# Kernel tuning notes

Hardware: AMD Instinct MI355X
Metric: run time of the kernel (lower is better)

Reference implementation:

```python
import jax, jax.numpy as jnp
import numpy as np
from jax import lax

NUM_ITER = 10
SMOOTH = 1.0
CL_WEIGHT = 0.5


def _min_pool(x, wh, ww):
    # torch: -max_pool2d(-x) pads with -inf -> min-pool with +inf boundary
    return lax.reduce_window(x, jnp.inf, lax.min,
                             (1, 1, wh, ww), (1, 1, 1, 1),
                             [(0, 0), (0, 0), (wh // 2, wh // 2), (ww // 2, ww // 2)])


def _max_pool(x, wh, ww):
    return lax.reduce_window(x, -jnp.inf, lax.max,
                             (1, 1, wh, ww), (1, 1, 1, 1),
                             [(0, 0), (0, 0), (wh // 2, wh // 2), (ww // 2, ww // 2)])


def soft_erode(img):
    return jnp.minimum(_min_pool(img, 3, 1), _min_pool(img, 1, 3))


def soft_dilate(img):
    return _max_pool(img, 3, 3)


def soft_open(img):
    return soft_dilate(soft_erode(img))


def soft_skeleton(img, num_iter=NUM_ITER):
    # img: (B,1,H,W)
    skel = jax.nn.relu(img - soft_open(img))

    def body(i, carry):
        img_e, skel = carry
        img_e = soft_erode(img_e)
        delta = jax.nn.relu(img_e - soft_open(img_e))
        skel = skel + jax.nn.relu(delta - skel * delta)
        return (img_e, skel)

    _, skel = lax.fori_loop(0, num_iter, body, (img, skel))
    return skel


def soft_dice(pred, target, smooth=SMOOTH):
    inter = jnp.sum(pred * target)
    return (2.0 * inter + smooth) / (jnp.sum(pred) + jnp.sum(target) + smooth)


def setup_inputs() -> dict:
    key = jax.random.key(0)
    k1, k2 = jax.random.split(key)
    pred = jax.random.normal(k1, (8, 1, 1024, 1024), dtype=jnp.float32)
    target = jax.random.randint(k2, (8, 1, 1024, 1024), 0, 2, dtype=jnp.int32)
    return {"pred": pred, "target": target}


def reference(pred, target):
    pred_prob = jax.nn.sigmoid(pred)          # (B,1,H,W)
    target_f = target.astype(pred_prob.dtype)

    skel_pred = soft_skeleton(pred_prob)
    skel_target = soft_skeleton(target_f)

    tprec = (jnp.sum(skel_pred * target_f) + SMOOTH) / (jnp.sum(skel_pred) + SMOOTH)
    tsens = (jnp.sum(skel_target * pred_prob) + SMOOTH) / (jnp.sum(skel_target) + SMOOTH)
    cl_dice = 2.0 * tprec * tsens / (tprec + tsens + 1e-7)

    dice = soft_dice(pred_prob, target_f)
    combined = (1.0 - CL_WEIGHT) * dice + CL_WEIGHT * cl_dice
    loss = 1.0 - combined
    return loss
```

## Files before the change

### kernel.cpp

```cpp
#include <hip/hip_runtime.h>
#include <math.h>

#define IMG  1024
#define TILE 64
#define HALO 12
#define SPP  52
#define NPRED (90*SPP)
#define SEN2 0x40004000u

typedef _Float16 h2 __attribute__((ext_vector_type(2)));
union UH { unsigned u; h2 h; };
__device__ __forceinline__ h2 u2h(unsigned u){ UH x; x.u=u; return x.h; }
__device__ __forceinline__ unsigned h2u(h2 h){ UH x; x.h=h; return x.u; }
__device__ __forceinline__ h2 pmin(h2 a, h2 b){ return __builtin_elementwise_min(a,b); }
__device__ __forceinline__ h2 pmax(h2 a, h2 b){ return __builtin_elementwise_max(a,b); }
__device__ __forceinline__ h2 funnel(h2 hi_src, h2 lo_src){
  return u2h((h2u(lo_src)>>16) | (h2u(hi_src)<<16));
}
__device__ __forceinline__ float sigmoidf(float x){ return 1.0f/(1.0f+__expf(-x)); }
__device__ __forceinline__ h2 unsent(h2 x, h2 onev, h2 zerov){
  h2 t = pmax(x-onev, zerov); return x - t - t;
}
__device__ __forceinline__ unsigned extract8(unsigned w0, unsigned w1, unsigned w2, int bp){
  unsigned long long lo = (unsigned long long)w0 | ((unsigned long long)w1<<32);
  unsigned long long hi = (unsigned long long)w1 | ((unsigned long long)w2<<32);
  unsigned a = (unsigned)(lo >> bp);
  unsigned b = (unsigned)(hi >> (bp & 31));
  return ((bp < 32) ? a : b) & 0xFFu;
}
__device__ __forceinline__ uint4 erode5(uint4 rm, uint4 rc, uint4 rn, h2 lw, h2 rv){
  h2 a0=u2h(rc.x), a1=u2h(rc.y), a2=u2h(rc.z), a3=u2h(rc.w);
  h2 v0=pmin(u2h(rm.x), u2h(rn.x));
  h2 v1=pmin(u2h(rm.y), u2h(rn.y));
  h2 v2=pmin(u2h(rm.z), u2h(rn.z));
  h2 v3=pmin(u2h(rm.w), u2h(rn.w));
  h2 f0=funnel(a0,lw), f1=funnel(a1,a0), f2=funnel(a2,a1), f3=funnel(a3,a2), f4=funnel(rv,a3);
  uint4 e;
  e.x=h2u(pmin(pmin(f0,f1),pmin(v0,a0)));
  e.y=h2u(pmin(pmin(f1,f2),pmin(v1,a1)));
  e.z=h2u(pmin(pmin(f2,f3),pmin(v2,a2)));
  e.w=h2u(pmin(pmin(f3,f4),pmin(v3,a3)));
  return e;
}

template<bool BND>
__device__ void pipeline(const float* __restrict__ pred, const int* __restrict__ targ,
                         long base, int gr0, int gc0, int tid,
                         unsigned* P, unsigned* Ta,
                         h2 val[8], h2 skel[8], unsigned &tbits, unsigned &skbits) {
  for (int i = tid; i < 104; i += 256) {
    int r = (i < 52) ? 0 : 89, c = (i < 52) ? i : i - 52;
    P[r*SPP + c] = SEN2;
  }
  for (int i = tid; i < 704; i += 256) {
    int r = 1 + (i >> 3), w = i & 7;
    w = (w < 2) ? w : 44 + w;
    P[r*SPP + w] = SEN2;
  }
  if (!BND) {
    #pragma unroll
    for (int k=0;k<4;++k){
      int u = tid + (k<<8);
      if (u < 968){
        int r = u/11, q = u - r*11;
        long g = base + (long)(gr0+r)*IMG + gc0 + (q<<3);
        float4 pa = *(const float4*)(pred+g);
        float4 pb = *(const float4*)(pred+g+4);
        h2 w0 = {(_Float16)sigmoidf(pa.x), (_Float16)sigmoidf(pa.y)};
        h2 w1 = {(_Float16)sigmoidf(pa.z), (_Float16)sigmoidf(pa.w)};
        h2 w2 = {(_Float16)sigmoidf(pb.x), (_Float16)sigmoidf(pb.y)};
        h2 w3 = {(_Float16)sigmoidf(pb.z), (_Float16)sigmoidf(pb.w)};
        int o = (1+r)*SPP + 2 + (q<<2);
        uint2 d0; d0.x=h2u(w0); d0.y=h2u(w1);
        uint2 d1; d1.x=h2u(w2); d1.y=h2u(w3);
        *(uint2*)&P[o]   = d0;
        *(uint2*)&P[o+2] = d1;
      }
    }
    #pragma unroll
    for (int k=0;k<2;++k){
      int u = tid + (k<<8);
      if (u < 264){
        int r = u/3, w = u - r*3;
        long g = base + (long)(gr0+r)*IMG + gc0 + (w<<5);
        unsigned bits = 0;
        #pragma unroll
        for (int i=0;i<8;++i){
          if (w < 2 || i < 6) {
            int4 tv = *(const int4*)(targ + g + (i<<2));
            unsigned nib = (unsigned)(tv.x!=0) | ((unsigned)(tv.y!=0)<<1)
                         | ((unsigned)(tv.z!=0)<<2) | ((unsigned)(tv.w!=0)<<3);
            bits |= nib << (i<<2);
          }
        }
        if (w==2) bits |= 0xFF000000u;
        Ta[u] = bits;
      }
    }
  } else {
    for (int i=tid; i<88*44; i+=256){
      int r = i/44, wd = i - r*44;
      int gr = gr0 + r;
      bool rok = (unsigned)gr < (unsigned)IMG;
      int gca = gc0 + (wd<<1), gcb = gca + 1;
      _Float16 va = (_Float16)2.0f, vb = (_Float16)2.0f;
      if (rok && (unsigned)gca < (unsigned)IMG) va = (_Float16)sigmoidf(pred[base + (long)gr*IMG + gca]);
      if (rok && (unsigned)gcb < (unsigned)IMG) vb = (_Float16)sigmoidf(pred[base + (long)gr*IMG + gcb]);
      h2 w; w.x = va; w.y = vb;
      P[(1+r)*SPP + 2 + wd] = h2u(w);
    }
    for (int u=tid; u<264; u+=256){
      int r = u/3, w = u - r*3;
      int gr = gr0 + r;
      bool rok = (unsigned)gr < (unsigned)IMG;
      unsigned bits = 0;
      for (int b=0;b<32;++b){
        int c = (w<<5) + b;
        unsigned bit = 1;
        if (c < 88) {
          int gc = gc0 + c;
          if (rok && (unsigned)gc < (unsigned)IMG) bit = (unsigned)(targ[base+(long)gr*IMG+gc] != 0);
        }
        bits |= bit << b;
      }
      Ta[u] = bits;
    }
  }
  __syncthreads();

  unsigned cm0=~0u, cm1=~0u, cm2=0x00FFFFFFu;
  bool colO = false;
  if (BND) {
    int lo = (-gc0 > 0) ? -gc0 : 0;
    int hi = (IMG - gc0 < 88) ? (IMG - gc0) : 88;
    colO = (lo > 0) || (hi < 88);
    unsigned m[3];
    #pragma unroll
    for (int w=0; w<3; ++w){
      int l = lo - (w<<5); if (l<0) l=0;
      int h = hi - (w<<5); if (h>32) h=32;
      unsigned mm = 0;
      if (h > l) {
        unsigned top = (h>=32)? ~0u : ((1u<<h)-1u);
        unsigned bot = (l<=0)? 0u : ((1u<<l)-1u);
        mm = top & ~bot;
      }
      m[w]=mm;
    }
    cm0=m[0]; cm1=m[1]; cm2=m[2] & 0x00FFFFFF;
  }

  const bool eact0 = (tid < 216);
  const int es = tid / 12, eq = tid - es*12;
  const int s5 = es * 5;
  const int ew = eq << 2;
  const int to = 3 + tid;
  const int twd = tid - (tid/3)*3;
  const bool tex = (tid < 2);
  const int to2 = 259 + tid;
  const int twd2 = (256+tid) - ((256+tid)/3)*3;

  const int qc = tid & 7;
  const int rg = tid >> 3;
  const int r0 = HALO + (rg<<1);
  const int wq = 8 + (qc<<2);
  const int bp = 12 + (qc<<3);

  h2 ep[8];
  {
    uint4 a0 = *(const uint4*)&P[(r0+1)*SPP + wq];
    uint4 a1 = *(const uint4*)&P[(r0+2)*SPP + wq];
    ep[0]=u2h(a0.x); ep[1]=u2h(a0.y); ep[2]=u2h(a0.z); ep[3]=u2h(a0.w);
    ep[4]=u2h(a1.x); ep[5]=u2h(a1.y); ep[6]=u2h(a1.z); ep[7]=u2h(a1.w);
    #pragma unroll
    for (int i=0;i<8;++i){ val[i]=ep[i]; skel[i]=(h2)(_Float16)0.0f; }
  }
  {
    int oa = r0*3, ob = (r0+1)*3;
    tbits = extract8(Ta[oa],Ta[oa+1],Ta[oa+2],bp)
          | (extract8(Ta[ob],Ta[ob+1],Ta[ob+2],bp) << 8);
  }
  unsigned tp0=0,tp1=0,tp2=0, sk0=0,sk1=0,sk2=0;
  const bool td = (tid < 64);
  const int tro = (12 + tid)*3;
  if (td) { tp0=Ta[tro]; tp1=Ta[tro+1]; tp2=Ta[tro+2]; }

  const h2 onev  = {(_Float16)1.0f,(_Float16)1.0f};
  const h2 zerov = {(_Float16)0.0f,(_Float16)0.0f};

  for (int j=0;j<11;++j){
    uint4 e[5];
    const bool act = eact0 && (s5+4 >= j+1) && (s5 <= 86-j);
    if (act){
      uint4 rm = *(const uint4*)&P[s5*SPP + ew];
      uint4 rc = *(const uint4*)&P[(s5+1)*SPP + ew];
      #pragma unroll
      for (int t=0;t<5;++t){
        int brn = s5 + 2 + t; brn = (brn > 89) ? 89 : brn;
        uint4 rn = *(const uint4*)&P[brn*SPP + ew];
        int brc = s5 + 1 + t; brc = (brc > 89) ? 89 : brc;
        h2 lw = u2h(P[brc*SPP + ew - 1]);
        h2 rv = u2h(P[brc*SPP + ew + 4]);
        e[t] = erode5(rm, rc, rn, lw, rv);
        rm = rc; rc = rn;
      }
    }
    unsigned tres, tres2;
    {
      unsigned own=Ta[to], up=Ta[to-3], dn=Ta[to+3];
      unsigned le = (twd>0)? Ta[to-1] : ~0u;
      unsigned ri = (twd<2)? Ta[to+1] : ~0u;
      unsigned h = own & ((own>>1)|(ri<<31)) & ((own<<1)|(le>>31));
      tres = h & up & dn;
    }
    if (tex){
      unsigned own=Ta[to2], up=Ta[to2-3], dn=Ta[to2+3];
      unsigned le = (twd2>0)? Ta[to2-1] : ~0u;
      unsigned ri = (twd2<2)? Ta[to2+1] : ~0u;
      unsigned h = own & ((own>>1)|(ri<<31)) & ((own<<1)|(le>>31));
      tres2 = h & up & dn;
    }
    __syncthreads();
    if (act){
      #pragma unroll
      for (int t=0;t<5;++t){
        int br = s5 + 1 + t; br = (br > 89) ? 89 : br;
        *(uint4*)&P[br*SPP + ew] = e[t];
      }
    }
    Ta[to] = tres;
    if (tex) Ta[to2] = tres2;
    __syncthreads();

    if (BND) {
      if (gr0 < 0) {
        for (int i=tid;i<12*44;i+=256){ int r=i/44; P[(1+r)*SPP+2+(i-r*44)] = SEN2; }
        if (tid < 36) Ta[tid] = ~0u;
      }
      if (gr0 + 88 > IMG) {
        for (int i=tid;i<12*44;i+=256){ int r=i/44; P[(77+r)*SPP+2+(i-r*44)] = SEN2; }
        if (tid < 36) Ta[228+tid] = ~0u;
      }
      if (colO) {
        if (gc0 < 0)
          for (int i=tid;i<88*6;i+=256){ int r=i/6; P[(1+r)*SPP+2+(i-r*6)] = SEN2; }
        if (gc0 + 88 > IMG)
          for (int i=tid;i<88*6;i+=256){ int r=i/6; P[(1+r)*SPP+40+(i-r*6)] = SEN2; }
        for (int i=tid;i<264;i+=256){
          int r=i/3, w=i-r*3;
          unsigned nm = (w==0)?~cm0:((w==1)?~cm1:~cm2);
          Ta[i] |= nm;
        }
      }
      __syncthreads();
    }

    h2 H[4][4];
    uint4 cap0, cap1;
    #pragma unroll
    for (int k=0;k<4;++k){
      int ro = (r0+k)*SPP + wq;
      uint4 c = *(const uint4*)&P[ro];
      h2 lwv = u2h(P[ro-1]);
      h2 rwv = u2h(P[ro+4]);
      if (k==1) cap0 = c;
      if (k==2) cap1 = c;
      h2 a0=u2h(c.x),a1=u2h(c.y),a2=u2h(c.z),a3=u2h(c.w);
      if (BND){
        a0=unsent(a0,onev,zerov); a1=unsent(a1,onev,zerov);
        a2=unsent(a2,onev,zerov); a3=unsent(a3,onev,zerov);
        lwv=unsent(lwv,onev,zerov); rwv=unsent(rwv,onev,zerov);
      }
      h2 f0=funnel(a0,lwv), f1=funnel(a1,a0), f2=funnel(a2,a1), f3=funnel(a3,a2), f4=funnel(rwv,a3);
      H[k][0]=pmax(pmax(f0,f1),a0);
      H[k][1]=pmax(pmax(f1,f2),a1);
      H[k][2]=pmax(pmax(f2,f3),a2);
      H[k][3]=pmax(pmax(f3,f4),a3);
    }
    #pragma unroll
    for (int i=0;i<4;++i){
      h2 m0 = pmax(pmax(H[0][i],H[1][i]),H[2][i]);
      h2 m1 = pmax(pmax(H[1][i],H[2][i]),H[3][i]);
      h2 d0 = pmax(ep[i]-m0, zerov);
      h2 d1 = pmax(ep[4+i]-m1, zerov);
      h2 x0 = d0 - skel[i]*d0;
      h2 x1 = d1 - skel[4+i]*d1;
      skel[i]   = skel[i]   + pmax(x0, zerov);
      skel[4+i] = skel[4+i] + pmax(x1, zerov);
    }
    ep[0]=u2h(cap0.x); ep[1]=u2h(cap0.y); ep[2]=u2h(cap0.z); ep[3]=u2h(cap0.w);
    ep[4]=u2h(cap1.x); ep[5]=u2h(cap1.y); ep[6]=u2h(cap1.z); ep[7]=u2h(cap1.w);

    if (td) {
      unsigned o0=Ta[tro], o1=Ta[tro+1], o2=Ta[tro+2];
      unsigned u0=Ta[tro-3], u1=Ta[tro-2], u2=Ta[tro-1];
      unsigned n0=Ta[tro+3], n1=Ta[tro+4], n2=Ta[tro+5];
      unsigned v0,v1,v2;
      if (BND){
        unsigned mu = ((unsigned)(gr0 + 11 + tid) < (unsigned)IMG) ? ~0u : 0u;
        unsigned md = ((unsigned)(gr0 + 13 + tid) < (unsigned)IMG) ? ~0u : 0u;
        v0 = ((u0&mu)|o0|(n0&md)) & cm0;
        v1 = ((u1&mu)|o1|(n1&md)) & cm1;
        v2 = ((u2&mu)|o2|(n2&md)) & cm2;
      } else {
        v0 = u0|o0|n0; v1 = u1|o1|n1; v2 = u2|o2|n2;
      }
      unsigned d0 = v0 | (v0<<1) | (v0>>1) | (v1<<31);
      unsigned d1 = v1 | (v1<<1) | (v0>>31) | (v1>>1) | (v2<<31);
      unsigned d2 = v2 | (v2<<1) | (v1>>31) | (v2>>1);
      sk0 |= tp0 & ~d0;
      sk1 |= tp1 & ~d1;
      sk2 |= tp2 & ~d2;
      tp0 = o0; tp1 = o1; tp2 = o2;
    }
  }

  __syncthreads();
  if (td){ Ta[3*tid]=sk0; Ta[3*tid+1]=sk1; Ta[3*tid+2]=sk2; }
  __syncthreads();
  {
    int o = (r0-12)*3;
    skbits = extract8(Ta[o],Ta[o+1],Ta[o+2],bp)
           | (extract8(Ta[o+3],Ta[o+4],Ta[o+5],bp) << 8);
  }
}

__global__ __launch_bounds__(256,4)
void cl_dice_main(const float* __restrict__ pred, const int* __restrict__ targ,
                  float* __restrict__ ws) {
  __shared__ alignas(16) unsigned sP[NPRED];
  __shared__ unsigned sTA[264];
  const int tid = threadIdx.x;
  const int gr0 = blockIdx.y * TILE - HALO;
  const int gc0 = blockIdx.x * TILE - HALO;
  const long base = (long)blockIdx.z * (long)(IMG * IMG);

  h2 val[8], skel[8]; unsigned tbits, skbits;
  const bool bnd = (blockIdx.x == 0) | (blockIdx.x == gridDim.x - 1) |
                   (blockIdx.y == 0) | (blockIdx.y == gridDim.y - 1);
  if (!bnd) pipeline<false>(pred, targ, base, gr0, gc0, tid, sP, sTA, val, skel, tbits, skbits);
  else      pipeline<true >(pred, targ, base, gr0, gc0, tid, sP, sTA, val, skel, tbits, skbits);

  float s[7] = {0,0,0,0,0,0,0};
  #pragma unroll
  for (int k=0;k<8;++k){
    int bb = ((k>>2)<<3) + ((k&3)<<1);
    float p0=(float)val[k].x,  p1=(float)val[k].y;
    float a0=(float)skel[k].x, a1=(float)skel[k].y;
    float t0=(float)((tbits>>bb)&1u),  t1=(float)((tbits>>(bb+1))&1u);
    float b0=(float)((skbits>>bb)&1u), b1=(float)((skbits>>(bb+1))&1u);
    s[0]+=a0+a1;        s[1]+=a0*t0+a1*t1;
    s[2]+=b0+b1;        s[3]+=b0*p0+b1*p1;
    s[4]+=p0*t0+p1*t1;  s[5]+=p0+p1;  s[6]+=t0+t1;
  }

  float* red = (float*)sP;
  #pragma unroll
  for (int k=0;k<7;++k){
    float v = s[k];
    v += __shfl_down(v,32); v += __shfl_down(v,16); v += __shfl_down(v,8);
    v += __shfl_down(v,4);  v += __shfl_down(v,2);  v += __shfl_down(v,1);
    if ((tid & 63) == 0) red[(tid>>6)*8 + k] = v;
  }
  __syncthreads();
  if (tid < 7) {
    float v = red[tid] + red[8+tid] + red[16+tid] + red[24+tid];
    int blk = (blockIdx.z * gridDim.y + blockIdx.y) * gridDim.x + blockIdx.x;
    ws[blk*8 + tid] = v;
  }
}

__global__ __launch_bounds__(256)
void cl_dice_finalize(const float* __restrict__ ws, float* __restrict__ out, int nblk) {
  __shared__ float red[4][8];
  int tid = threadIdx.x;
  float acc[7] = {0,0,0,0,0,0,0};
  for (int i=tid; i<nblk; i+=256) {
    #pragma unroll
    for (int k=0;k<7;++k) acc[k] += ws[i*8 + k];
  }
  #pragma unroll
  for (int k=0;k<7;++k){
    float v = acc[k];
    v += __shfl_down(v,32); v += __shfl_down(v,16); v += __shfl_down(v,8);
    v += __shfl_down(v,4);  v += __shfl_down(v,2);  v += __shfl_down(v,1);
    if ((tid & 63) == 0) red[tid>>6][k] = v;
  }
  __syncthreads();
  if (tid == 0) {
    float t0[7];
    #pragma unroll
    for (int k=0;k<7;++k) t0[k] = red[0][k] + red[1][k] + red[2][k] + red[3][k];
    float sum_sp = t0[0], sum_spt = t0[1], sum_st = t0[2], sum_stp = t0[3];
    float inter  = t0[4], sum_p   = t0[5], sum_t  = t0[6];
    float tprec = (sum_spt + 1.0f) / (sum_sp + 1.0f);
    float tsens = (sum_stp + 1.0f) / (sum_st + 1.0f);
    float cl    = 2.0f * tprec * tsens / (tprec + tsens + 1e-7f);
    float dice  = (2.0f * inter + 1.0f) / (sum_p + sum_t + 1.0f);
    out[0] = 1.0f - 0.5f * (dice + cl);
  }
}

extern "C" void kernel_launch(void* const* d_in, const int* in_sizes, int n_in,
                              void* d_out, int out_size, void* d_ws, size_t ws_size,
                              hipStream_t stream) {
  const float* pred = (const float*)d_in[0];
  const int*   targ = (const int*)d_in[1];
  float* ws  = (float*)d_ws;
  float* out = (float*)d_out;

  const int B = in_sizes[0] / (IMG * IMG);
  dim3 grid(IMG / TILE, IMG / TILE, B);
  cl_dice_main<<<grid, 256, 0, stream>>>(pred, targ, ws);

  const int nblk = (IMG / TILE) * (IMG / TILE) * B;
  cl_dice_finalize<<<1, 256, 0, stream>>>(ws, out, nblk);
}
```

Measured before the change: 247.7 us.

## Double-buffer LDS erosion planes to drop a barrier per iteration

The shared-memory prediction tile and target bitmap are now ping-pong buffered (A/B and Ta/Tb). Erosion results are written straight into the other buffer instead of being held in registers until a barrier, so one __syncthreads per skeleton iteration goes away and register pressure drops. Column-based activity masks also skip erosion work on halo columns that no longer affect the output as the valid region shrinks. The cost is twice the LDS per block, which may limit how many blocks fit on a CU, and the skipped regions now hold stale halo data.

```diff
diff --git a/kernel.cpp b/kernel.cpp
--- a/kernel.cpp
+++ b/kernel.cpp
@@ -46,16 +46,16 @@
 template<bool BND>
 __device__ void pipeline(const float* __restrict__ pred, const int* __restrict__ targ,
                          long base, int gr0, int gc0, int tid,
-                         unsigned* P, unsigned* Ta,
+                         unsigned* A, unsigned* B, unsigned* Ta, unsigned* Tb,
                          h2 val[8], h2 skel[8], unsigned &tbits, unsigned &skbits) {
   for (int i = tid; i < 104; i += 256) {
     int r = (i < 52) ? 0 : 89, c = (i < 52) ? i : i - 52;
-    P[r*SPP + c] = SEN2;
+    A[r*SPP + c] = SEN2;  B[r*SPP + c] = SEN2;
   }
   for (int i = tid; i < 704; i += 256) {
     int r = 1 + (i >> 3), w = i & 7;
     w = (w < 2) ? w : 44 + w;
-    P[r*SPP + w] = SEN2;
+    A[r*SPP + w] = SEN2;  B[r*SPP + w] = SEN2;
   }
   if (!BND) {
     #pragma unroll
@@ -73,8 +73,8 @@
         int o = (1+r)*SPP + 2 + (q<<2);
         uint2 d0; d0.x=h2u(w0); d0.y=h2u(w1);
         uint2 d1; d1.x=h2u(w2); d1.y=h2u(w3);
-        *(uint2*)&P[o]   = d0;
-        *(uint2*)&P[o+2] = d1;
+        *(uint2*)&A[o]   = d0;
+        *(uint2*)&A[o+2] = d1;
       }
     }
     #pragma unroll
@@ -107,7 +107,7 @@
       if (rok && (unsigned)gca < (unsigned)IMG) va = (_Float16)sigmoidf(pred[base + (long)gr*IMG + gca]);
       if (rok && (unsigned)gcb < (unsigned)IMG) vb = (_Float16)sigmoidf(pred[base + (long)gr*IMG + gcb]);
       h2 w; w.x = va; w.y = vb;
-      P[(1+r)*SPP + 2 + wd] = h2u(w);
+      A[(1+r)*SPP + 2 + wd] = h2u(w);
     }
     for (int u=tid; u<264; u+=256){
       int r = u/3, w = u - r*3;
@@ -154,6 +154,8 @@
   const int es = tid / 12, eq = tid - es*12;
   const int s5 = es * 5;
   const int ew = eq << 2;
+  const int c_lo = (eq<<3) + 3;
+  const int c_hi = (eq<<3) - 4;
   const int to = 3 + tid;
   const int twd = tid - (tid/3)*3;
   const bool tex = (tid < 2);
@@ -168,8 +170,8 @@
 
   h2 ep[8];
   {
-    uint4 a0 = *(const uint4*)&P[(r0+1)*SPP + wq];
-    uint4 a1 = *(const uint4*)&P[(r0+2)*SPP + wq];
+    uint4 a0 = *(const uint4*)&A[(r0+1)*SPP + wq];
+    uint4 a1 = *(const uint4*)&A[(r0+2)*SPP + wq];
     ep[0]=u2h(a0.x); ep[1]=u2h(a0.y); ep[2]=u2h(a0.z); ep[3]=u2h(a0.w);
     ep[4]=u2h(a1.x); ep[5]=u2h(a1.y); ep[6]=u2h(a1.z); ep[7]=u2h(a1.w);
     #pragma unroll
@@ -189,67 +191,56 @@
   const h2 zerov = {(_Float16)0.0f,(_Float16)0.0f};
 
   for (int j=0;j<11;++j){
-    uint4 e[5];
-    const bool act = eact0 && (s5+4 >= j+1) && (s5 <= 86-j);
+    const bool act = eact0 && (s5+4 >= j+1) && (s5 <= 86-j)
+                           && (c_lo >= j+1) && (c_hi <= 86-j);
     if (act){
-      uint4 rm = *(const uint4*)&P[s5*SPP + ew];
-      uint4 rc = *(const uint4*)&P[(s5+1)*SPP + ew];
+      uint4 rm = *(const uint4*)&A[s5*SPP + ew];
+      uint4 rc = *(const uint4*)&A[(s5+1)*SPP + ew];
       #pragma unroll
       for (int t=0;t<5;++t){
         int brn = s5 + 2 + t; brn = (brn > 89) ? 89 : brn;
-        uint4 rn = *(const uint4*)&P[brn*SPP + ew];
+        uint4 rn = *(const uint4*)&A[brn*SPP + ew];
         int brc = s5 + 1 + t; brc = (brc > 89) ? 89 : brc;
-        h2 lw = u2h(P[brc*SPP + ew - 1]);
-        h2 rv = u2h(P[brc*SPP + ew + 4]);
-        e[t] = erode5(rm, rc, rn, lw, rv);
+        h2 lw = u2h(A[brc*SPP + ew - 1]);
+        h2 rv = u2h(A[brc*SPP + ew + 4]);
+        *(uint4*)&B[brc*SPP + ew] = erode5(rm, rc, rn, lw, rv);
         rm = rc; rc = rn;
       }
     }
-    unsigned tres, tres2;
     {
       unsigned own=Ta[to], up=Ta[to-3], dn=Ta[to+3];
       unsigned le = (twd>0)? Ta[to-1] : ~0u;
       unsigned ri = (twd<2)? Ta[to+1] : ~0u;
       unsigned h = own & ((own>>1)|(ri<<31)) & ((own<<1)|(le>>31));
-      tres = h & up & dn;
+      Tb[to] = h & up & dn;
     }
     if (tex){
       unsigned own=Ta[to2], up=Ta[to2-3], dn=Ta[to2+3];
       unsigned le = (twd2>0)? Ta[to2-1] : ~0u;
       unsigned ri = (twd2<2)? Ta[to2+1] : ~0u;
       unsigned h = own & ((own>>1)|(ri<<31)) & ((own<<1)|(le>>31));
-      tres2 = h & up & dn;
-    }
-    __syncthreads();
-    if (act){
-      #pragma unroll
-      for (int t=0;t<5;++t){
-        int br = s5 + 1 + t; br = (br > 89) ? 89 : br;
-        *(uint4*)&P[br*SPP + ew] = e[t];
-      }
-    }
-    Ta[to] = tres;
-    if (tex) Ta[to2] = tres2;
+      Tb[to2] = h & up & dn;
+    }
     __syncthreads();
 
     if (BND) {
       if (gr0 < 0) {
-        for (int i=tid;i<12*44;i+=256){ int r=i/44; P[(1+r)*SPP+2+(i-r*44)] = SEN2; }
-        if (tid < 36) Ta[tid] = ~0u;
+        for (int i=tid;i<12*44;i+=256){ int r=i/44; B[(1+r)*SPP+2+(i-r*44)] = SEN2; }
+        if (tid < 36) Tb[tid] = ~0u;
       }
       if (gr0 + 88 > IMG) {
-        for (int i=tid;i<12*44;i+=256){ int r=i/44; P[(77+r)*SPP+2+(i-r*44)] = SEN2; }
-        if (tid < 36) Ta[228+tid] = ~0u;
+        for (int i=tid;i<12*44;i+=256){ int r=i/44; B[(77+r)*SPP+2+(i-r*44)] = SEN2; }
+        if (tid < 36) Tb[228+tid] = ~0u;
       }
       if (colO) {
         if (gc0 < 0)
-          for (int i=tid;i<88*6;i+=256){ int r=i/6; P[(1+r)*SPP+2+(i-r*6)] = SEN2; }
+          for (int i=tid;i<88*6;i+=256){ int r=i/6; B[(1+r)*SPP+2+(i-r*6)] = SEN2; }
         if (gc0 + 88 > IMG)
-          for (int i=tid;i<88*6;i+=256){ int r=i/6; P[(1+r)*SPP+40+(i-r*6)] = SEN2; }
+          for (int i=tid;i<88*6;i+=256){ int r=i/6; B[(1+r)*SPP+40+(i-r*6)] = SEN2; }
         for (int i=tid;i<264;i+=256){
           int r=i/3, w=i-r*3;
           unsigned nm = (w==0)?~cm0:((w==1)?~cm1:~cm2);
-          Ta[i] |= nm;
+          Tb[i] |= nm;
         }
       }
       __syncthreads();
@@ -260,9 +251,9 @@
     #pragma unroll
     for (int k=0;k<4;++k){
       int ro = (r0+k)*SPP + wq;
-      uint4 c = *(const uint4*)&P[ro];
-      h2 lwv = u2h(P[ro-1]);
-      h2 rwv = u2h(P[ro+4]);
+      uint4 c = *(const uint4*)&B[ro];
+      h2 lwv = u2h(B[ro-1]);
+      h2 rwv = u2h(B[ro+4]);
       if (k==1) cap0 = c;
       if (k==2) cap1 = c;
       h2 a0=u2h(c.x),a1=u2h(c.y),a2=u2h(c.z),a3=u2h(c.w);
@@ -292,9 +283,9 @@
     ep[4]=u2h(cap1.x); ep[5]=u2h(cap1.y); ep[6]=u2h(cap1.z); ep[7]=u2h(cap1.w);
 
     if (td) {
-      unsigned o0=Ta[tro], o1=Ta[tro+1], o2=Ta[tro+2];
-      unsigned u0=Ta[tro-3], u1=Ta[tro-2], u2=Ta[tro-1];
-      unsigned n0=Ta[tro+3], n1=Ta[tro+4], n2=Ta[tro+5];
+      unsigned o0=Tb[tro], o1=Tb[tro+1], o2=Tb[tro+2];
+      unsigned u0=Tb[tro-3], u1=Tb[tro-2], u2=Tb[tro-1];
+      unsigned n0=Tb[tro+3], n1=Tb[tro+4], n2=Tb[tro+5];
       unsigned v0,v1,v2;
       if (BND){
         unsigned mu = ((unsigned)(gr0 + 11 + tid) < (unsigned)IMG) ? ~0u : 0u;
@@ -313,6 +304,8 @@
       sk2 |= tp2 & ~d2;
       tp0 = o0; tp1 = o1; tp2 = o2;
     }
+    unsigned* t1 = A;  A = B;  B = t1;
+    unsigned* t2 = Ta; Ta = Tb; Tb = t2;
   }
 
   __syncthreads();
@@ -328,8 +321,9 @@
 __global__ __launch_bounds__(256,4)
 void cl_dice_main(const float* __restrict__ pred, const int* __restrict__ targ,
                   float* __restrict__ ws) {
-  __shared__ alignas(16) unsigned sP[NPRED];
-  __shared__ unsigned sTA[264];
+  __shared__ alignas(16) unsigned sPA[NPRED];
+  __shared__ alignas(16) unsigned sPB[NPRED];
+  __shared__ unsigned sTA[264], sTB[264];
   const int tid = threadIdx.x;
   const int gr0 = blockIdx.y * TILE - HALO;
   const int gc0 = blockIdx.x * TILE - HALO;
@@ -338,8 +332,8 @@
   h2 val[8], skel[8]; unsigned tbits, skbits;
   const bool bnd = (blockIdx.x == 0) | (blockIdx.x == gridDim.x - 1) |
                    (blockIdx.y == 0) | (blockIdx.y == gridDim.y - 1);
-  if (!bnd) pipeline<false>(pred, targ, base, gr0, gc0, tid, sP, sTA, val, skel, tbits, skbits);
-  else      pipeline<true >(pred, targ, base, gr0, gc0, tid, sP, sTA, val, skel, tbits, skbits);
+  if (!bnd) pipeline<false>(pred, targ, base, gr0, gc0, tid, sPA, sPB, sTA, sTB, val, skel, tbits, skbits);
+  else      pipeline<true >(pred, targ, base, gr0, gc0, tid, sPA, sPB, sTA, sTB, val, skel, tbits, skbits);
 
   float s[7] = {0,0,0,0,0,0,0};
   #pragma unroll
@@ -354,7 +348,7 @@
     s[4]+=p0*t0+p1*t1;  s[5]+=p0+p1;  s[6]+=t0+t1;
   }
 
-  float* red = (float*)sP;
+  float* red = (float*)sPA;
   #pragma unroll
   for (int k=0;k<7;++k){
     float v = s[k];
```

Result: no change. 243.9 us, median of 2 (-1.5%).

## Widen tile to 128x64 to cut halo overhead per output pixel

Applied to the files above, without the earlier changes.

Changes the block tile from 64x64 to 128 columns by 64 rows, widening the shared buffers and remapping threads so each one handles 4 rows by 8 columns and erodes 8 rows per step. The aim is to shrink the ratio of 12-pixel halo recomputation and redundant loads to useful output, and to halve the number of blocks. In exchange each thread uses more registers (16 h2 values for val and skel each) and more shared memory, which may lower occupancy, and some threads sit idle in the erode stage.

```diff
diff --git a/kernel.cpp b/kernel.cpp
--- a/kernel.cpp
+++ b/kernel.cpp
@@ -2,10 +2,12 @@
 #include <math.h>
 
 #define IMG  1024
-#define TILE 64
+#define TC   128
+#define TR   64
 #define HALO 12
-#define SPP  52
+#define SPP  84
 #define NPRED (90*SPP)
+#define NTW  440
 #define SEN2 0x40004000u
 
 typedef _Float16 h2 __attribute__((ext_vector_type(2)));
@@ -21,12 +23,9 @@
 __device__ __forceinline__ h2 unsent(h2 x, h2 onev, h2 zerov){
   h2 t = pmax(x-onev, zerov); return x - t - t;
 }
-__device__ __forceinline__ unsigned extract8(unsigned w0, unsigned w1, unsigned w2, int bp){
-  unsigned long long lo = (unsigned long long)w0 | ((unsigned long long)w1<<32);
-  unsigned long long hi = (unsigned long long)w1 | ((unsigned long long)w2<<32);
-  unsigned a = (unsigned)(lo >> bp);
-  unsigned b = (unsigned)(hi >> (bp & 31));
-  return ((bp < 32) ? a : b) & 0xFFu;
+__device__ __forceinline__ unsigned ext8b(unsigned a, unsigned b, int sh){
+  unsigned long long v = ((unsigned long long)b<<32) | (unsigned long long)a;
+  return (unsigned)((v >> sh) & 0xFFull);
 }
 __device__ __forceinline__ uint4 erode5(uint4 rm, uint4 rc, uint4 rn, h2 lw, h2 rv){
   h2 a0=u2h(rc.x), a1=u2h(rc.y), a2=u2h(rc.z), a3=u2h(rc.w);
@@ -47,22 +46,22 @@
 __device__ void pipeline(const float* __restrict__ pred, const int* __restrict__ targ,
                          long base, int gr0, int gc0, int tid,
                          unsigned* P, unsigned* Ta,
-                         h2 val[8], h2 skel[8], unsigned &tbits, unsigned &skbits) {
-  for (int i = tid; i < 104; i += 256) {
-    int r = (i < 52) ? 0 : 89, c = (i < 52) ? i : i - 52;
+                         h2 val[16], h2 skel[16], unsigned &tbits, unsigned &skbits) {
+  for (int i = tid; i < 168; i += 256) {
+    int r = (i < 84) ? 0 : 89, c = (i < 84) ? i : i - 84;
     P[r*SPP + c] = SEN2;
   }
   for (int i = tid; i < 704; i += 256) {
     int r = 1 + (i >> 3), w = i & 7;
-    w = (w < 2) ? w : 44 + w;
+    w = (w < 2) ? w : 76 + w;
     P[r*SPP + w] = SEN2;
   }
   if (!BND) {
     #pragma unroll
-    for (int k=0;k<4;++k){
+    for (int k=0;k<7;++k){
       int u = tid + (k<<8);
-      if (u < 968){
-        int r = u/11, q = u - r*11;
+      if (u < 1672){
+        int r = u/19, q = u - r*19;
         long g = base + (long)(gr0+r)*IMG + gc0 + (q<<3);
         float4 pa = *(const float4*)(pred+g);
         float4 pb = *(const float4*)(pred+g+4);
@@ -80,26 +79,26 @@
     #pragma unroll
     for (int k=0;k<2;++k){
       int u = tid + (k<<8);
-      if (u < 264){
-        int r = u/3, w = u - r*3;
+      if (u < NTW){
+        int r = u/5, w = u - r*5;
         long g = base + (long)(gr0+r)*IMG + gc0 + (w<<5);
         unsigned bits = 0;
         #pragma unroll
         for (int i=0;i<8;++i){
-          if (w < 2 || i < 6) {
+          if (w < 4 || i < 6) {
             int4 tv = *(const int4*)(targ + g + (i<<2));
             unsigned nib = (unsigned)(tv.x!=0) | ((unsigned)(tv.y!=0)<<1)
                          | ((unsigned)(tv.z!=0)<<2) | ((unsigned)(tv.w!=0)<<3);
             bits |= nib << (i<<2);
           }
         }
-        if (w==2) bits |= 0xFF000000u;
+        if (w==4) bits |= 0xFF000000u;
         Ta[u] = bits;
       }
     }
   } else {
-    for (int i=tid; i<88*44; i+=256){
-      int r = i/44, wd = i - r*44;
+    for (int i=tid; i<88*76; i+=256){
+      int r = i/76, wd = i - r*76;
       int gr = gr0 + r;
       bool rok = (unsigned)gr < (unsigned)IMG;
       int gca = gc0 + (wd<<1), gcb = gca + 1;
@@ -109,15 +108,15 @@
       h2 w; w.x = va; w.y = vb;
       P[(1+r)*SPP + 2 + wd] = h2u(w);
     }
-    for (int u=tid; u<264; u+=256){
-      int r = u/3, w = u - r*3;
+    for (int u=tid; u<NTW; u+=256){
+      int r = u/5, w = u - r*5;
       int gr = gr0 + r;
       bool rok = (unsigned)gr < (unsigned)IMG;
       unsigned bits = 0;
       for (int b=0;b<32;++b){
         int c = (w<<5) + b;
         unsigned bit = 1;
-        if (c < 88) {
+        if (c < 152) {
           int gc = gc0 + c;
           if (rok && (unsigned)gc < (unsigned)IMG) bit = (unsigned)(targ[base+(long)gr*IMG+gc] != 0);
         }
@@ -128,15 +127,14 @@
   }
   __syncthreads();
 
-  unsigned cm0=~0u, cm1=~0u, cm2=0x00FFFFFFu;
+  unsigned cm[5] = {~0u,~0u,~0u,~0u,0x00FFFFFFu};
   bool colO = false;
   if (BND) {
     int lo = (-gc0 > 0) ? -gc0 : 0;
-    int hi = (IMG - gc0 < 88) ? (IMG - gc0) : 88;
-    colO = (lo > 0) || (hi < 88);
-    unsigned m[3];
-    #pragma unroll
-    for (int w=0; w<3; ++w){
+    int hi = (IMG - gc0 < 152) ? (IMG - gc0) : 152;
+    colO = (lo > 0) || (hi < 152);
+    #pragma unroll
+    for (int w=0; w<5; ++w){
       int l = lo - (w<<5); if (l<0) l=0;
       int h = hi - (w<<5); if (h>32) h=32;
       unsigned mm = 0;
@@ -145,126 +143,128 @@
         unsigned bot = (l<=0)? 0u : ((1u<<l)-1u);
         mm = top & ~bot;
       }
-      m[w]=mm;
-    }
-    cm0=m[0]; cm1=m[1]; cm2=m[2] & 0x00FFFFFF;
-  }
-
-  const bool eact0 = (tid < 216);
-  const int es = tid / 12, eq = tid - es*12;
-  const int s5 = es * 5;
+      cm[w] = mm;
+    }
+    cm[4] &= 0x00FFFFFFu;
+  }
+
+  const bool eact = (tid < 220);
+  const int es = tid / 20, eq = tid - es*20;
+  const int s8 = es << 3;
   const int ew = eq << 2;
-  const int to = 3 + tid;
-  const int twd = tid - (tid/3)*3;
-  const bool tex = (tid < 2);
-  const int to2 = 259 + tid;
-  const int twd2 = (256+tid) - ((256+tid)/3)*3;
-
-  const int qc = tid & 7;
-  const int rg = tid >> 3;
-  const int r0 = HALO + (rg<<1);
-  const int wq = 8 + (qc<<2);
-  const int bp = 12 + (qc<<3);
-
-  h2 ep[8];
-  {
-    uint4 a0 = *(const uint4*)&P[(r0+1)*SPP + wq];
-    uint4 a1 = *(const uint4*)&P[(r0+2)*SPP + wq];
-    ep[0]=u2h(a0.x); ep[1]=u2h(a0.y); ep[2]=u2h(a0.z); ep[3]=u2h(a0.w);
-    ep[4]=u2h(a1.x); ep[5]=u2h(a1.y); ep[6]=u2h(a1.z); ep[7]=u2h(a1.w);
-    #pragma unroll
-    for (int i=0;i<8;++i){ val[i]=ep[i]; skel[i]=(h2)(_Float16)0.0f; }
-  }
-  {
-    int oa = r0*3, ob = (r0+1)*3;
-    tbits = extract8(Ta[oa],Ta[oa+1],Ta[oa+2],bp)
-          | (extract8(Ta[ob],Ta[ob+1],Ta[ob+2],bp) << 8);
-  }
-  unsigned tp0=0,tp1=0,tp2=0, sk0=0,sk1=0,sk2=0;
+  const int cqh = (eq<<3) + 3;
+  const int cql = (eq<<3) - 4;
+  const int o1 = 5 + tid;
+  const int twd1 = tid - (tid/5)*5;
+  const bool t2 = (tid < 174);
+  const int o2 = 261 + tid;
+  const int twd2 = (tid+1) - ((tid+1)/5)*5;
+
+  const int qd = tid & 15;
+  const int rg = tid >> 4;
+  const int r0 = HALO + (rg<<2);
+  const int wq = 8 + (qd<<2);
+  const int bp = HALO + (qd<<3);
+  const int bw0 = bp >> 5, bsh = bp & 31;
+
+  h2 ep[16];
+  #pragma unroll
+  for (int r=0;r<4;++r){
+    uint4 c = *(const uint4*)&P[(r0+1+r)*SPP + wq];
+    ep[4*r+0]=u2h(c.x); ep[4*r+1]=u2h(c.y); ep[4*r+2]=u2h(c.z); ep[4*r+3]=u2h(c.w);
+  }
+  #pragma unroll
+  for (int i=0;i<16;++i){ val[i]=ep[i]; skel[i]=(h2)(_Float16)0.0f; }
+  tbits = 0;
+  #pragma unroll
+  for (int r=0;r<4;++r){
+    int row = r0 + r;
+    unsigned b2 = (bw0 < 4) ? Ta[5*row + bw0 + 1] : 0u;
+    tbits |= ext8b(Ta[5*row + bw0], b2, bsh) << (r<<3);
+  }
+  unsigned tp[5]={0,0,0,0,0}, sk[5]={0,0,0,0,0};
   const bool td = (tid < 64);
-  const int tro = (12 + tid)*3;
-  if (td) { tp0=Ta[tro]; tp1=Ta[tro+1]; tp2=Ta[tro+2]; }
+  const int tro = 5*(12 + tid);
+  if (td){ 
+    #pragma unroll
+    for (int w=0;w<5;++w) tp[w]=Ta[tro+w];
+  }
 
   const h2 onev  = {(_Float16)1.0f,(_Float16)1.0f};
   const h2 zerov = {(_Float16)0.0f,(_Float16)0.0f};
 
   for (int j=0;j<11;++j){
-    uint4 e[5];
-    const bool act = eact0 && (s5+4 >= j+1) && (s5 <= 86-j);
+    uint4 e[8];
+    const bool act = eact && (s8+7 >= j+1) && (s8 <= 86-j)
+                          && (cqh >= j+1) && (cql <= 150-j);
     if (act){
-      uint4 rm = *(const uint4*)&P[s5*SPP + ew];
-      uint4 rc = *(const uint4*)&P[(s5+1)*SPP + ew];
+      uint4 rm = *(const uint4*)&P[s8*SPP + ew];
+      uint4 rc = *(const uint4*)&P[(s8+1)*SPP + ew];
       #pragma unroll
-      for (int t=0;t<5;++t){
-        int brn = s5 + 2 + t; brn = (brn > 89) ? 89 : brn;
-        uint4 rn = *(const uint4*)&P[brn*SPP + ew];
-        int brc = s5 + 1 + t; brc = (brc > 89) ? 89 : brc;
-        h2 lw = u2h(P[brc*SPP + ew - 1]);
-        h2 rv = u2h(P[brc*SPP + ew + 4]);
+      for (int t=0;t<8;++t){
+        uint4 rn = *(const uint4*)&P[(s8+2+t)*SPP + ew];
+        h2 lw = u2h(P[(s8+1+t)*SPP + ew - 1]);
+        h2 rv = u2h(P[(s8+1+t)*SPP + ew + 4]);
         e[t] = erode5(rm, rc, rn, lw, rv);
         rm = rc; rc = rn;
       }
     }
-    unsigned tres, tres2;
+    unsigned tr1, tr2;
     {
-      unsigned own=Ta[to], up=Ta[to-3], dn=Ta[to+3];
-      unsigned le = (twd>0)? Ta[to-1] : ~0u;
-      unsigned ri = (twd<2)? Ta[to+1] : ~0u;
+      unsigned own=Ta[o1], up=Ta[o1-5], dn=Ta[o1+5];
+      unsigned le = (twd1>0)? Ta[o1-1] : ~0u;
+      unsigned ri = (twd1<4)? Ta[o1+1] : ~0u;
       unsigned h = own & ((own>>1)|(ri<<31)) & ((own<<1)|(le>>31));
-      tres = h & up & dn;
-    }
-    if (tex){
-      unsigned own=Ta[to2], up=Ta[to2-3], dn=Ta[to2+3];
-      unsigned le = (twd2>0)? Ta[to2-1] : ~0u;
-      unsigned ri = (twd2<2)? Ta[to2+1] : ~0u;
+      tr1 = h & up & dn;
+    }
+    if (t2){
+      unsigned own=Ta[o2], up=Ta[o2-5], dn=Ta[o2+5];
+      unsigned le = (twd2>0)? Ta[o2-1] : ~0u;
+      unsigned ri = (twd2<4)? Ta[o2+1] : ~0u;
       unsigned h = own & ((own>>1)|(ri<<31)) & ((own<<1)|(le>>31));
-      tres2 = h & up & dn;
+      tr2 = h & up & dn;
     }
     __syncthreads();
     if (act){
       #pragma unroll
-      for (int t=0;t<5;++t){
-        int br = s5 + 1 + t; br = (br > 89) ? 89 : br;
-        *(uint4*)&P[br*SPP + ew] = e[t];
-      }
-    }
-    Ta[to] = tres;
-    if (tex) Ta[to2] = tres2;
+      for (int t=0;t<8;++t)
+        *(uint4*)&P[(s8+1+t)*SPP + ew] = e[t];
+    }
+    Ta[o1] = tr1;
+    if (t2) Ta[o2] = tr2;
     __syncthreads();
 
     if (BND) {
       if (gr0 < 0) {
-        for (int i=tid;i<12*44;i+=256){ int r=i/44; P[(1+r)*SPP+2+(i-r*44)] = SEN2; }
-        if (tid < 36) Ta[tid] = ~0u;
+        for (int i=tid;i<912;i+=256){ int r=i/76; P[(1+r)*SPP+2+(i-r*76)] = SEN2; }
+        if (tid < 60) Ta[tid] = ~0u;
       }
       if (gr0 + 88 > IMG) {
-        for (int i=tid;i<12*44;i+=256){ int r=i/44; P[(77+r)*SPP+2+(i-r*44)] = SEN2; }
-        if (tid < 36) Ta[228+tid] = ~0u;
+        for (int i=tid;i<912;i+=256){ int r=i/76; P[(77+r)*SPP+2+(i-r*76)] = SEN2; }
+        if (tid < 60) Ta[380+tid] = ~0u;
       }
       if (colO) {
         if (gc0 < 0)
-          for (int i=tid;i<88*6;i+=256){ int r=i/6; P[(1+r)*SPP+2+(i-r*6)] = SEN2; }
-        if (gc0 + 88 > IMG)
-          for (int i=tid;i<88*6;i+=256){ int r=i/6; P[(1+r)*SPP+40+(i-r*6)] = SEN2; }
-        for (int i=tid;i<264;i+=256){
-          int r=i/3, w=i-r*3;
-          unsigned nm = (w==0)?~cm0:((w==1)?~cm1:~cm2);
-          Ta[i] |= nm;
+          for (int i=tid;i<528;i+=256){ int r=i/6; P[(1+r)*SPP+2+(i-r*6)] = SEN2; }
+        if (gc0 + 152 > IMG)
+          for (int i=tid;i<528;i+=256){ int r=i/6; P[(1+r)*SPP+72+(i-r*6)] = SEN2; }
+        for (int i=tid;i<NTW;i+=256){
+          int r=i/5, w=i-r*5;
+          Ta[i] |= ~cm[w];
         }
       }
       __syncthreads();
     }
 
-    h2 H[4][4];
-    uint4 cap0, cap1;
-    #pragma unroll
-    for (int k=0;k<4;++k){
+    h2 H[6][4];
+    uint4 cap[4];
+    #pragma unroll
+    for (int k=0;k<6;++k){
       int ro = (r0+k)*SPP + wq;
       uint4 c = *(const uint4*)&P[ro];
       h2 lwv = u2h(P[ro-1]);
       h2 rwv = u2h(P[ro+4]);
-      if (k==1) cap0 = c;
-      if (k==2) cap1 = c;
+      if (k>=1 && k<=4) cap[k-1] = c;
       h2 a0=u2h(c.x),a1=u2h(c.y),a2=u2h(c.z),a3=u2h(c.w);
       if (BND){
         a0=unsent(a0,onev,zerov); a1=unsent(a1,onev,zerov);
@@ -278,50 +278,58 @@
       H[k][3]=pmax(pmax(f3,f4),a3);
     }
     #pragma unroll
-    for (int i=0;i<4;++i){
-      h2 m0 = pmax(pmax(H[0][i],H[1][i]),H[2][i]);
-      h2 m1 = pmax(pmax(H[1][i],H[2][i]),H[3][i]);
-      h2 d0 = pmax(ep[i]-m0, zerov);
-      h2 d1 = pmax(ep[4+i]-m1, zerov);
-      h2 x0 = d0 - skel[i]*d0;
-      h2 x1 = d1 - skel[4+i]*d1;
-      skel[i]   = skel[i]   + pmax(x0, zerov);
-      skel[4+i] = skel[4+i] + pmax(x1, zerov);
-    }
-    ep[0]=u2h(cap0.x); ep[1]=u2h(cap0.y); ep[2]=u2h(cap0.z); ep[3]=u2h(cap0.w);
-    ep[4]=u2h(cap1.x); ep[5]=u2h(cap1.y); ep[6]=u2h(cap1.z); ep[7]=u2h(cap1.w);
+    for (int r=0;r<4;++r){
+      #pragma unroll
+      for (int i=0;i<4;++i){
+        h2 m = pmax(pmax(H[r][i],H[r+1][i]),H[r+2][i]);
+        h2 d = pmax(ep[4*r+i]-m, zerov);
+        h2 x = d - skel[4*r+i]*d;
+        skel[4*r+i] = skel[4*r+i] + pmax(x, zerov);
+      }
+    }
+    #pragma unroll
+    for (int r=0;r<4;++r){
+      ep[4*r+0]=u2h(cap[r].x); ep[4*r+1]=u2h(cap[r].y);
+      ep[4*r+2]=u2h(cap[r].z); ep[4*r+3]=u2h(cap[r].w);
+    }
 
     if (td) {
-      unsigned o0=Ta[tro], o1=Ta[tro+1], o2=Ta[tro+2];
-      unsigned u0=Ta[tro-3], u1=Ta[tro-2], u2=Ta[tro-1];
-      unsigned n0=Ta[tro+3], n1=Ta[tro+4], n2=Ta[tro+5];
-      unsigned v0,v1,v2;
+      unsigned o[5], u[5], n[5], v[5];
+      #pragma unroll
+      for (int w=0;w<5;++w){ o[w]=Ta[tro+w]; u[w]=Ta[tro-5+w]; n[w]=Ta[tro+5+w]; }
       if (BND){
         unsigned mu = ((unsigned)(gr0 + 11 + tid) < (unsigned)IMG) ? ~0u : 0u;
         unsigned md = ((unsigned)(gr0 + 13 + tid) < (unsigned)IMG) ? ~0u : 0u;
-        v0 = ((u0&mu)|o0|(n0&md)) & cm0;
-        v1 = ((u1&mu)|o1|(n1&md)) & cm1;
-        v2 = ((u2&mu)|o2|(n2&md)) & cm2;
+        #pragma unroll
+        for (int w=0;w<5;++w) v[w] = ((u[w]&mu)|o[w]|(n[w]&md)) & cm[w];
       } else {
-        v0 = u0|o0|n0; v1 = u1|o1|n1; v2 = u2|o2|n2;
-      }
-      unsigned d0 = v0 | (v0<<1) | (v0>>1) | (v1<<31);
-      unsigned d1 = v1 | (v1<<1) | (v0>>31) | (v1>>1) | (v2<<31);
-      unsigned d2 = v2 | (v2<<1) | (v1>>31) | (v2>>1);
-      sk0 |= tp0 & ~d0;
-      sk1 |= tp1 & ~d1;
-      sk2 |= tp2 & ~d2;
-      tp0 = o0; tp1 = o1; tp2 = o2;
+        #pragma unroll
+        for (int w=0;w<5;++w) v[w] = u[w]|o[w]|n[w];
+      }
+      unsigned d0 = v[0] | (v[0]<<1) | (v[0]>>1) | (v[1]<<31);
+      unsigned d1 = v[1] | (v[1]<<1) | (v[0]>>31) | (v[1]>>1) | (v[2]<<31);
+      unsigned d2 = v[2] | (v[2]<<1) | (v[1]>>31) | (v[2]>>1) | (v[3]<<31);
+      unsigned d3 = v[3] | (v[3]<<1) | (v[2]>>31) | (v[3]>>1) | (v[4]<<31);
+      unsigned d4 = v[4] | (v[4]<<1) | (v[3]>>31) | (v[4]>>1);
+      sk[0] |= tp[0] & ~d0;  sk[1] |= tp[1] & ~d1;  sk[2] |= tp[2] & ~d2;
+      sk[3] |= tp[3] & ~d3;  sk[4] |= tp[4] & ~d4;
+      #pragma unroll
+      for (int w=0;w<5;++w) tp[w] = o[w];
     }
   }
 
   __syncthreads();
-  if (td){ Ta[3*tid]=sk0; Ta[3*tid+1]=sk1; Ta[3*tid+2]=sk2; }
+  if (td){
+    #pragma unroll
+    for (int w=0;w<5;++w) Ta[5*tid+w] = sk[w];
+  }
   __syncthreads();
-  {
-    int o = (r0-12)*3;
-    skbits = extract8(Ta[o],Ta[o+1],Ta[o+2],bp)
-           | (extract8(Ta[o+3],Ta[o+4],Ta[o+5],bp) << 8);
+  skbits = 0;
+  #pragma unroll
+  for (int r=0;r<4;++r){
+    int row = (rg<<2) + r;
+    unsigned b2 = (bw0 < 4) ? Ta[5*row + bw0 + 1] : 0u;
+    skbits |= ext8b(Ta[5*row + bw0], b2, bsh) << (r<<3);
   }
 }
 
@@ -329,13 +337,13 @@
 void cl_dice_main(const float* __restrict__ pred, const int* __restrict__ targ,
                   float* __restrict__ ws) {
   __shared__ alignas(16) unsigned sP[NPRED];
-  __shared__ unsigned sTA[264];
+  __shared__ unsigned sTA[NTW];
   const int tid = threadIdx.x;
-  const int gr0 = blockIdx.y * TILE - HALO;
-  const int gc0 = blockIdx.x * TILE - HALO;
+  const int gr0 = blockIdx.y * TR - HALO;
+  const int gc0 = blockIdx.x * TC - HALO;
   const long base = (long)blockIdx.z * (long)(IMG * IMG);
 
-  h2 val[8], skel[8]; unsigned tbits, skbits;
+  h2 val[16], skel[16]; unsigned tbits, skbits;
   const bool bnd = (blockIdx.x == 0) | (blockIdx.x == gridDim.x - 1) |
                    (blockIdx.y == 0) | (blockIdx.y == gridDim.y - 1);
   if (!bnd) pipeline<false>(pred, targ, base, gr0, gc0, tid, sP, sTA, val, skel, tbits, skbits);
@@ -343,7 +351,7 @@
 
   float s[7] = {0,0,0,0,0,0,0};
   #pragma unroll
-  for (int k=0;k<8;++k){
+  for (int k=0;k<16;++k){
     int bb = ((k>>2)<<3) + ((k&3)<<1);
     float p0=(float)val[k].x,  p1=(float)val[k].y;
     float a0=(float)skel[k].x, a1=(float)skel[k].y;
@@ -410,9 +418,9 @@
   float* out = (float*)d_out;
 
   const int B = in_sizes[0] / (IMG * IMG);
-  dim3 grid(IMG / TILE, IMG / TILE, B);
+  dim3 grid(IMG / TC, IMG / TR, B);
   cl_dice_main<<<grid, 256, 0, stream>>>(pred, targ, ws);
 
-  const int nblk = (IMG / TILE) * (IMG / TILE) * B;
+  const int nblk = (IMG / TC) * (IMG / TR) * B;
   cl_dice_finalize<<<1, 256, 0, stream>>>(ws, out, nblk);
 }
```

Measured after the change: 271.6 us. +9.7%, slower.
